# Optimization experiments

Hardware: AMD Instinct MI355X
Metric: run time of the kernel (lower is better)

## Reference

```python
import jax, jax.numpy as jnp
import numpy as np

N_SRC, N_DST, E = 65536, 16384, 262144
IN, HID, H = 256, 128, 4
N_POI, K = 100000, 50
NEG_SLOPE = 0.2


def setup_inputs() -> dict:
    key = jax.random.key(0)
    ks = jax.random.split(key, 13)
    feat = jax.random.normal(ks[0], (N_SRC, IN), jnp.float32)
    poi_cat_feat = jax.random.normal(ks[1], (N_POI, IN), jnp.float32)
    poi_coeff = jax.random.uniform(ks[2], (N_POI, K), jnp.float32)
    fc_w = jax.random.normal(ks[3], (H * HID, IN), jnp.float32) * 0.05
    attn_l = jax.random.normal(ks[4], (H, HID), jnp.float32) * 0.05
    attn_r = jax.random.normal(ks[5], (H, HID), jnp.float32) * 0.05
    bias_p = jnp.zeros((H * HID,), jnp.float32)
    res_w = jax.random.normal(ks[6], (H * HID, IN), jnp.float32) * 0.05
    w_w = jax.random.normal(ks[7], (HID, IN), jnp.float32) * 0.05
    src_idx = jax.random.randint(ks[8], (E,), 0, N_SRC)
    dst_idx = jax.random.randint(ks[9], (E,), 0, N_DST)
    output_nodes = jax.random.randint(ks[10], (N_DST,), 0, N_POI)
    neighbor_counts = jax.random.randint(ks[11], (N_POI,), 1, K + 1)
    return dict(feat=feat, poi_cat_feat=poi_cat_feat, poi_coeff=poi_coeff,
                fc_w=fc_w, attn_l=attn_l, attn_r=attn_r, bias_p=bias_p,
                res_w=res_w, w_w=w_w, src_idx=src_idx, dst_idx=dst_idx,
                output_nodes=output_nodes, neighbor_counts=neighbor_counts)


def reference(feat, poi_cat_feat, poi_coeff, fc_w, attn_l, attn_r, bias_p,
              res_w, w_w, src_idx, dst_idx, output_nodes, neighbor_counts):
    # ---- DGL GATConv on block (src -> dst), feat_drop/attn_drop = 0 (eval) ----
    feat_src = (feat @ fc_w.T).reshape(N_SRC, H, HID)        # [Nsrc,H,D]
    el = jnp.einsum('nhd,hd->nh', feat_src, attn_l)          # [Nsrc,H]
    er = jnp.einsum('nhd,hd->nh', feat_src[:N_DST], attn_r)  # [Ndst,H]
    e = jax.nn.leaky_relu(el[src_idx] + er[dst_idx], NEG_SLOPE)  # [E,H]
    # edge softmax per destination node (numerically stable)
    m = jax.ops.segment_max(e, dst_idx, num_segments=N_DST)
    m = jnp.where(jnp.isfinite(m), m, 0.0)
    ex = jnp.exp(e - m[dst_idx])
    denom = jax.ops.segment_sum(ex, dst_idx, num_segments=N_DST)
    a = ex / jnp.maximum(denom[dst_idx], 1e-9)               # [E,H]
    msgs = a[:, :, None] * feat_src[src_idx]                 # [E,H,D]
    rst = jax.ops.segment_sum(msgs, dst_idx, num_segments=N_DST)  # [Ndst,H,D]
    res = (feat[:N_DST] @ res_w.T).reshape(N_DST, H, HID)    # residual projection
    feat_gat = jax.nn.elu(rst + res + bias_p.reshape(1, H, HID))
    # ---- per-node neighbor-weighted sum: sum_j beta[nid,j] * W @ poi_cat_feat[nid],
    #      over first min(count,50) neighbors (cap-50 padded mask) ----
    cf = poi_cat_feat[output_nodes]                          # [Ndst,IN]
    valid = (jnp.arange(K)[None, :] < neighbor_counts[output_nodes][:, None])
    s = jnp.sum(poi_coeff[output_nodes] * valid.astype(cf.dtype), axis=-1)  # [Ndst]
    feat_dist = (cf @ w_w.T) * s[:, None]                    # [Ndst,HID]
    out = jax.nn.relu((feat_gat + feat_dist[:, None, :]) / 2)
    return out
```

## Files before the change

### kernel.cpp

```cpp
#include <hip/hip_runtime.h>

#define N_SRC 65536
#define N_DST 16384
#define NEDGE 262144
#define FIN 256
#define HID 128
#define KNB 50
#define NEG 0.2f
#define BCAP 64

typedef short bf8 __attribute__((ext_vector_type(8)));
typedef float f32x4 __attribute__((ext_vector_type(4)));

static __device__ __forceinline__ short f2bf(float f) {
    union { float f; unsigned u; } v; v.f = f;
    unsigned r = v.u + 0x7fffu + ((v.u >> 16) & 1u);
    return (short)(r >> 16);
}
static __device__ __forceinline__ float bf2f(short b) {
    union { unsigned u; float f; } v; v.u = ((unsigned)(unsigned short)b) << 16;
    return v.f;
}

static __device__ __forceinline__ unsigned char f2e4(float f) {
    union { float f; unsigned u; } v; v.f = f;
    unsigned s = (v.u >> 24) & 0x80u;
    v.u &= 0x7FFFFFFFu;
    v.f = fminf(v.f, 240.0f);
    unsigned u = v.u + 0x00080000u;
    int eb = (int)(u >> 23) - 120;
    if (eb < 1) return (unsigned char)s;
    unsigned m = (u >> 20) & 7u;
    return (unsigned char)(s | ((unsigned)eb << 3) | m);
}

__global__ __launch_bounds__(256) void k_prep_all(
    const float* __restrict__ feat, short* __restrict__ feat_bf,
    const float* __restrict__ fc, const float* __restrict__ rw,
    const float* __restrict__ ww, short* __restrict__ fco,
    short* __restrict__ rwo, short* __restrict__ wwo,
    const float* __restrict__ poi, const float* __restrict__ poi_coeff,
    const int* __restrict__ nodes, const int* __restrict__ ncounts,
    short* __restrict__ cf, float* __restrict__ sArr,
    const int* __restrict__ src_idx, const int* __restrict__ dst_idx,
    int* __restrict__ counts, int* __restrict__ bucket) {
    int b = blockIdx.x;
    if (b < 16384) {
        int i = b * 256 + threadIdx.x;
        float4 v = ((const float4*)feat)[i];
        short4 o; o.x = f2bf(v.x); o.y = f2bf(v.y); o.z = f2bf(v.z); o.w = f2bf(v.w);
        ((short4*)feat_bf)[i] = o;
    } else if (b < 16672) {
        int i = (b - 16384) * 256 + threadIdx.x;
        const float* src; short* dst; int off;
        if (i < 32768) { src = fc; dst = fco; off = i; }
        else if (i < 65536) { src = rw; dst = rwo; off = i - 32768; }
        else { src = ww; dst = wwo; off = i - 65536; }
        float4 v = ((const float4*)src)[off];
        short4 o; o.x = f2bf(v.x); o.y = f2bf(v.y); o.z = f2bf(v.z); o.w = f2bf(v.w);
        ((short4*)dst)[off] = o;
    } else if (b < 20768) {
        int wv = threadIdx.x >> 6, lane = threadIdx.x & 63;
        int row = (b - 16672) * 4 + wv;
        int nid = nodes[row];
        float4 v = ((const float4*)(poi + (size_t)nid * FIN))[lane];
        short4 o; o.x = f2bf(v.x); o.y = f2bf(v.y); o.z = f2bf(v.z); o.w = f2bf(v.w);
        ((short4*)(cf + (size_t)row * FIN))[lane] = o;
        int cnt = ncounts[nid];
        float s = (lane < cnt && lane < KNB) ? poi_coeff[(size_t)nid * KNB + lane] : 0.f;
        for (int m = 1; m < 64; m <<= 1) s += __shfl_xor(s, m);
        if (lane == 0) sArr[row] = s;
    } else {
        int e = (b - 20768) * 256 + threadIdx.x;
        int d = dst_idx[e];
        int pos = atomicAdd(&counts[d], 1);
        if (pos < BCAP) bucket[d * BCAP + pos] = src_idx[e];
    }
}

__global__ __launch_bounds__(256, 3) void k_gemm_all(
    const short* __restrict__ feat_bf, const short* __restrict__ fcw,
    const short* __restrict__ resw, const short* __restrict__ ww,
    const short* __restrict__ cf_bf, unsigned char* __restrict__ feat_src8,
    short* __restrict__ resO, short* __restrict__ fdist,
    const float* __restrict__ sArr, const float* __restrict__ attn_l,
    const float* __restrict__ attn_r, float* __restrict__ el, float* __restrict__ er) {
    __shared__ __align__(16) short Abuf[128 * 64];
    __shared__ __align__(16) short Bbuf[128 * 64];
    int b0 = blockIdx.x;
    int b = (b0 & 7) * 336 + (b0 >> 3);
    const short *A, *W; const float* scale = nullptr;
    short* C16 = nullptr;
    int N = 512, do_elr = 0, rowBase, colBase;
    if (b < 2048) {
        A = feat_bf; W = fcw; do_elr = 1;
        colBase = (b & 3) * 128; rowBase = (b >> 2) * 128;
    } else if (b < 2560) {
        int bb = b - 2048;
        A = feat_bf; W = resw; C16 = resO;
        colBase = (bb & 3) * 128; rowBase = (bb >> 2) * 128;
    } else {
        int bb = b - 2560;
        A = cf_bf; W = ww; C16 = fdist; scale = sArr; N = 128;
        colBase = 0; rowBase = bb * 128;
    }
    int t = threadIdx.x, wv = t >> 6, lane = t & 63;
    int l15 = lane & 15, quad = lane >> 4;
    const short* sbase = (wv < 2) ? (A + (size_t)rowBase * FIN)
                                  : (W + (size_t)colBase * FIN);
    short* dbase = (wv < 2) ? Abuf : Bbuf;
    int s0 = (wv & 1) * 8;
    int rsub = lane >> 3;
    int cg = (lane & 7) ^ rsub;

    f32x4 acc[2][8] = {};
    for (int kb = 0; kb < 4; kb++) {
#pragma unroll
        for (int q = 0; q < 8; q++) {
            int slab = s0 + q;
            int r_loc = slab * 8 + rsub;
            __builtin_amdgcn_global_load_lds(
                (const __attribute__((address_space(1))) void*)(sbase + (size_t)r_loc * FIN + kb * 64 + cg * 8),
                (__attribute__((address_space(3))) void*)(dbase + slab * 512), 16, 0, 0);
        }
        asm volatile("s_waitcnt vmcnt(0)" ::: "memory");
        __syncthreads();
#pragma unroll
        for (int kk = 0; kk < 2; kk++) {
            int gidx = (quad + kk * 4) ^ (l15 & 7);
            bf8 a[2], bfr[8];
#pragma unroll
            for (int i = 0; i < 2; i++) {
                int row = wv * 32 + i * 16 + l15;
                a[i] = *(const bf8*)(Abuf + (row * 8 + gidx) * 8);
            }
#pragma unroll
            for (int j = 0; j < 8; j++) {
                int row = j * 16 + l15;
                bfr[j] = *(const bf8*)(Bbuf + (row * 8 + gidx) * 8);
            }
#pragma unroll
            for (int i = 0; i < 2; i++)
#pragma unroll
                for (int j = 0; j < 8; j++)
                    acc[i][j] = __builtin_amdgcn_mfma_f32_16x16x32_bf16(a[i], bfr[j], acc[i][j], 0, 0, 0);
        }
        if (kb < 3) __syncthreads();
    }
#pragma unroll
    for (int i = 0; i < 2; i++)
#pragma unroll
        for (int r = 0; r < 4; r++) {
            int row = rowBase + wv * 32 + i * 16 + quad * 4 + r;
            if (do_elr) {
#pragma unroll
                for (int j = 0; j < 8; j++)
                    feat_src8[(size_t)row * 512 + colBase + j * 16 + l15] = f2e4(acc[i][j][r]);
            } else {
                float sc = scale ? scale[row] : 1.0f;
#pragma unroll
                for (int j = 0; j < 8; j++)
                    C16[(size_t)row * N + colBase + j * 16 + l15] = f2bf(acc[i][j][r] * sc);
            }
        }
    if (do_elr) {
        int h = colBase >> 7;
        float alv[8], arv[8];
#pragma unroll
        for (int j = 0; j < 8; j++) {
            alv[j] = attn_l[h * HID + j * 16 + l15];
            arv[j] = attn_r[h * HID + j * 16 + l15];
        }
#pragma unroll
        for (int i = 0; i < 2; i++)
#pragma unroll
            for (int r = 0; r < 4; r++) {
                float dl = 0.f, dr = 0.f;
#pragma unroll
                for (int j = 0; j < 8; j++) {
                    float c = acc[i][j][r];
                    dl += c * alv[j];
                    dr += c * arv[j];
                }
                dl += __shfl_xor(dl, 1); dr += __shfl_xor(dr, 1);
                dl += __shfl_xor(dl, 2); dr += __shfl_xor(dr, 2);
                dl += __shfl_xor(dl, 4); dr += __shfl_xor(dr, 4);
                dl += __shfl_xor(dl, 8); dr += __shfl_xor(dr, 8);
                if (l15 == 0) {
                    int row = rowBase + wv * 32 + i * 16 + quad * 4 + r;
                    el[row * 4 + h] = dl;
                    if (row < N_DST) er[row * 4 + h] = dr;
                }
            }
    }
}

__global__ __launch_bounds__(256) void k_agg(const int* __restrict__ counts,
                                             const int* __restrict__ bucket,
                                             const float* __restrict__ el,
                                             const float* __restrict__ er,
                                             const unsigned char* __restrict__ feat_src8,
                                             const short* __restrict__ res,
                                             const float* __restrict__ bias,
                                             const short* __restrict__ fdist,
                                             float* __restrict__ out) {
    __shared__ __align__(16) float aSm[4][256];
    __shared__ int sSm[4][64];
    int wv = threadIdx.x >> 6, lane = threadIdx.x & 63;
    int d = blockIdx.x * 4 + wv;
    int cnt = counts[d]; cnt = cnt < BCAP ? cnt : BCAP;
    float4 erv = *(const float4*)(er + (size_t)d * 4);

    int srow = 0;
    float v0 = -1e30f, v1 = -1e30f, v2 = -1e30f, v3 = -1e30f;
    if (lane < cnt) {
        srow = bucket[d * BCAP + lane];
        float4 lv = *(const float4*)(el + (size_t)srow * 4);
        v0 = lv.x + erv.x; v0 = v0 > 0 ? v0 : NEG * v0;
        v1 = lv.y + erv.y; v1 = v1 > 0 ? v1 : NEG * v1;
        v2 = lv.z + erv.z; v2 = v2 > 0 ? v2 : NEG * v2;
        v3 = lv.w + erv.w; v3 = v3 > 0 ? v3 : NEG * v3;
    }
    float m0 = v0, m1 = v1, m2 = v2, m3 = v3;
    for (int sh = 1; sh < 64; sh <<= 1) {
        m0 = fmaxf(m0, __shfl_xor(m0, sh)); m1 = fmaxf(m1, __shfl_xor(m1, sh));
        m2 = fmaxf(m2, __shfl_xor(m2, sh)); m3 = fmaxf(m3, __shfl_xor(m3, sh));
    }
    float e0 = 0.f, e1 = 0.f, e2 = 0.f, e3 = 0.f;
    if (lane < cnt) {
        e0 = __expf(v0 - m0); e1 = __expf(v1 - m1);
        e2 = __expf(v2 - m2); e3 = __expf(v3 - m3);
    }
    float s0 = e0, s1 = e1, s2 = e2, s3 = e3;
    for (int sh = 1; sh < 64; sh <<= 1) {
        s0 += __shfl_xor(s0, sh); s1 += __shfl_xor(s1, sh);
        s2 += __shfl_xor(s2, sh); s3 += __shfl_xor(s3, sh);
    }
    const float S = 0x1p120f;
    float i0 = S / fmaxf(s0, 1e-9f), i1 = S / fmaxf(s1, 1e-9f);
    float i2 = S / fmaxf(s2, 1e-9f), i3 = S / fmaxf(s3, 1e-9f);
    *(float4*)&aSm[wv][lane * 4] = make_float4(e0 * i0, e1 * i1, e2 * i2, e3 * i3);
    sSm[wv][lane] = srow;
    asm volatile("s_waitcnt lgkmcnt(0)" ::: "memory");

    int myh = lane >> 4, col0 = lane * 8;
    float acc[8] = {0.f, 0.f, 0.f, 0.f, 0.f, 0.f, 0.f, 0.f};
    for (int c = 0; c < cnt; c++) {
        int srw = sSm[wv][c];
        float afs = aSm[wv][c * 4 + myh];
        const unsigned char* p = feat_src8 + ((size_t)srw << 9) + col0;
        uint2 w8 = *(const uint2*)p;
#pragma unroll
        for (int j = 0; j < 4; j++) {
            unsigned blo = (w8.x >> (8 * j)) & 0xFFu;
            unsigned bhi = (w8.y >> (8 * j)) & 0xFFu;
            union { unsigned u; float f; } xl, xh;
            xl.u = ((blo & 0x80u) << 24) | ((blo & 0x7Fu) << 20);
            xh.u = ((bhi & 0x80u) << 24) | ((bhi & 0x7Fu) << 20);
            acc[j]     = fmaf(afs, xl.f, acc[j]);
            acc[j + 4] = fmaf(afs, xh.f, acc[j + 4]);
        }
    }

    bf8 rv = *(const bf8*)(res + (size_t)d * 512 + col0);
    float4 bv0 = *(const float4*)(bias + col0);
    float4 bv1 = *(const float4*)(bias + col0 + 4);
    float bb[8] = {bv0.x, bv0.y, bv0.z, bv0.w, bv1.x, bv1.y, bv1.z, bv1.w};
    bf8 fv = *(const bf8*)(fdist + (size_t)d * HID + (col0 & 127));
    float o[8];
#pragma unroll
    for (int j = 0; j < 8; j++) {
        float g = acc[j] + bf2f(rv[j]) + bb[j];
        g = g > 0 ? g : expm1f(g);
        float v = (g + bf2f(fv[j])) * 0.5f;
        o[j] = v > 0 ? v : 0.f;
    }
    float* op = out + (size_t)d * 512 + col0;
    *(float4*)op = make_float4(o[0], o[1], o[2], o[3]);
    *(float4*)(op + 4) = make_float4(o[4], o[5], o[6], o[7]);
}

extern "C" void kernel_launch(void* const* d_in, const int* in_sizes, int n_in,
                              void* d_out, int out_size, void* d_ws, size_t ws_size,
                              hipStream_t stream) {
    const float* feat      = (const float*)d_in[0];
    const float* poi_cat   = (const float*)d_in[1];
    const float* poi_coeff = (const float*)d_in[2];
    const float* fc_w      = (const float*)d_in[3];
    const float* attn_l    = (const float*)d_in[4];
    const float* attn_r    = (const float*)d_in[5];
    const float* bias_p    = (const float*)d_in[6];
    const float* res_w     = (const float*)d_in[7];
    const float* w_w       = (const float*)d_in[8];
    const int* src_idx     = (const int*)d_in[9];
    const int* dst_idx     = (const int*)d_in[10];
    const int* out_nodes   = (const int*)d_in[11];
    const int* ncounts     = (const int*)d_in[12];
    float* out = (float*)d_out;

    char* w = (char*)d_ws;
    auto alloc = [&](size_t bytes) -> char* {
        char* p = w; w += (bytes + 255) & ~(size_t)255; return p;
    };
    short* feat_bf  = (short*)alloc((size_t)N_SRC * FIN * 2);
    short* fcw_bf   = (short*)alloc((size_t)512 * FIN * 2);
    short* resw_bf  = (short*)alloc((size_t)512 * FIN * 2);
    short* ww_bf    = (short*)alloc((size_t)HID * FIN * 2);
    short* cf_bf    = (short*)alloc((size_t)N_DST * FIN * 2);
    unsigned char* feat_src8 = (unsigned char*)alloc((size_t)N_SRC * 512);
    short* res      = (short*)alloc((size_t)N_DST * 512 * 2);
    short* fdist    = (short*)alloc((size_t)N_DST * HID * 2);
    float* el       = (float*)alloc((size_t)N_SRC * 4 * 4);
    float* er       = (float*)alloc((size_t)N_DST * 4 * 4);
    float* sArr     = (float*)alloc((size_t)N_DST * 4);
    int* counts     = (int*)alloc((size_t)N_DST * 4);
    int* bucket     = (int*)alloc((size_t)N_DST * BCAP * 4);

    hipMemsetAsync(counts, 0, N_DST * 4, stream);

    k_prep_all<<<21792, 256, 0, stream>>>(feat, feat_bf, fc_w, res_w, w_w,
                                          fcw_bf, resw_bf, ww_bf,
                                          poi_cat, poi_coeff, out_nodes, ncounts,
                                          cf_bf, sArr, src_idx, dst_idx,
                                          counts, bucket);

    k_gemm_all<<<2688, 256, 0, stream>>>(feat_bf, fcw_bf, resw_bf, ww_bf, cf_bf,
                                         feat_src8, res, fdist, sArr,
                                         attn_l, attn_r, el, er);

    k_agg<<<N_DST / 4, 256, 0, stream>>>(counts, bucket, el, er,
                                         feat_src8, res, bias_p, fdist, out);
}
```

Before: 308.0 us.

## Fuse memset, prep, GEMM and aggregation into one cooperative persistent kernel

Replaces the memset plus three separate kernel launches with a single cooperative persistent kernel. It sizes the grid to resident capacity, loops each block over virtual block indices, and separates the phases with grid-wide syncs. This is meant to remove launch overhead and inter-kernel gaps and tail drain. In exchange it adds grid.sync costs, and the persistent loops may balance work less well than hardware scheduling. A fallback path keeps the original multi-kernel launches if the cooperative launch is unavailable.

Measured after the change: 305.3 us. About the same (-0.9%).

```diff
diff --git a/kernel.cpp b/kernel.cpp
--- a/kernel.cpp
+++ b/kernel.cpp
@@ -1,4 +1,7 @@
 #include <hip/hip_runtime.h>
+#include <hip/hip_cooperative_groups.h>
+
+namespace cgrp = cooperative_groups;
 
 #define N_SRC 65536
 #define N_DST 16384
@@ -34,84 +37,77 @@
     return (unsigned char)(s | ((unsigned)eb << 3) | m);
 }
 
-__global__ __launch_bounds__(256) void k_prep_all(
-    const float* __restrict__ feat, short* __restrict__ feat_bf,
-    const float* __restrict__ fc, const float* __restrict__ rw,
-    const float* __restrict__ ww, short* __restrict__ fco,
-    short* __restrict__ rwo, short* __restrict__ wwo,
-    const float* __restrict__ poi, const float* __restrict__ poi_coeff,
-    const int* __restrict__ nodes, const int* __restrict__ ncounts,
-    short* __restrict__ cf, float* __restrict__ sArr,
-    const int* __restrict__ src_idx, const int* __restrict__ dst_idx,
-    int* __restrict__ counts, int* __restrict__ bucket) {
-    int b = blockIdx.x;
-    if (b < 16384) {
-        int i = b * 256 + threadIdx.x;
-        float4 v = ((const float4*)feat)[i];
+struct MegaP {
+    const float *feat, *poi, *coeff, *attnl, *attnr, *bias;
+    const float *fc32, *rw32, *ww32;
+    const int *src, *dst, *nodes, *ncnt;
+    short *feat_bf, *fcw, *resw, *ww, *cf;
+    unsigned char *fsrc8;
+    short *res, *fdist;
+    float *el, *er, *sArr, *out;
+    int *counts, *bucket;
+};
+
+
+static __device__ __forceinline__ void dev_prep(int vb, int t, const MegaP& P) {
+    if (vb < 16384) {
+        int i = vb * 256 + t;
+        float4 v = ((const float4*)P.feat)[i];
         short4 o; o.x = f2bf(v.x); o.y = f2bf(v.y); o.z = f2bf(v.z); o.w = f2bf(v.w);
-        ((short4*)feat_bf)[i] = o;
-    } else if (b < 16672) {
-        int i = (b - 16384) * 256 + threadIdx.x;
+        ((short4*)P.feat_bf)[i] = o;
+    } else if (vb < 16672) {
+        int i = (vb - 16384) * 256 + t;
         const float* src; short* dst; int off;
-        if (i < 32768) { src = fc; dst = fco; off = i; }
-        else if (i < 65536) { src = rw; dst = rwo; off = i - 32768; }
-        else { src = ww; dst = wwo; off = i - 65536; }
+        if (i < 32768) { src = P.fc32; dst = P.fcw; off = i; }
+        else if (i < 65536) { src = P.rw32; dst = P.resw; off = i - 32768; }
+        else { src = P.ww32; dst = P.ww; off = i - 65536; }
         float4 v = ((const float4*)src)[off];
         short4 o; o.x = f2bf(v.x); o.y = f2bf(v.y); o.z = f2bf(v.z); o.w = f2bf(v.w);
         ((short4*)dst)[off] = o;
-    } else if (b < 20768) {
-        int wv = threadIdx.x >> 6, lane = threadIdx.x & 63;
-        int row = (b - 16672) * 4 + wv;
-        int nid = nodes[row];
-        float4 v = ((const float4*)(poi + (size_t)nid * FIN))[lane];
+    } else if (vb < 20768) {
+        int wv = t >> 6, lane = t & 63;
+        int row = (vb - 16672) * 4 + wv;
+        int nid = P.nodes[row];
+        float4 v = ((const float4*)(P.poi + (size_t)nid * FIN))[lane];
         short4 o; o.x = f2bf(v.x); o.y = f2bf(v.y); o.z = f2bf(v.z); o.w = f2bf(v.w);
-        ((short4*)(cf + (size_t)row * FIN))[lane] = o;
-        int cnt = ncounts[nid];
-        float s = (lane < cnt && lane < KNB) ? poi_coeff[(size_t)nid * KNB + lane] : 0.f;
+        ((short4*)(P.cf + (size_t)row * FIN))[lane] = o;
+        int cnt = P.ncnt[nid];
+        float s = (lane < cnt && lane < KNB) ? P.coeff[(size_t)nid * KNB + lane] : 0.f;
         for (int m = 1; m < 64; m <<= 1) s += __shfl_xor(s, m);
-        if (lane == 0) sArr[row] = s;
+        if (lane == 0) P.sArr[row] = s;
     } else {
-        int e = (b - 20768) * 256 + threadIdx.x;
-        int d = dst_idx[e];
-        int pos = atomicAdd(&counts[d], 1);
-        if (pos < BCAP) bucket[d * BCAP + pos] = src_idx[e];
-    }
-}
-
-__global__ __launch_bounds__(256, 3) void k_gemm_all(
-    const short* __restrict__ feat_bf, const short* __restrict__ fcw,
-    const short* __restrict__ resw, const short* __restrict__ ww,
-    const short* __restrict__ cf_bf, unsigned char* __restrict__ feat_src8,
-    short* __restrict__ resO, short* __restrict__ fdist,
-    const float* __restrict__ sArr, const float* __restrict__ attn_l,
-    const float* __restrict__ attn_r, float* __restrict__ el, float* __restrict__ er) {
-    __shared__ __align__(16) short Abuf[128 * 64];
-    __shared__ __align__(16) short Bbuf[128 * 64];
-    int b0 = blockIdx.x;
-    int b = (b0 & 7) * 336 + (b0 >> 3);
+        int e = (vb - 20768) * 256 + t;
+        int d = P.dst[e];
+        int pos = atomicAdd(&P.counts[d], 1);
+        if (pos < BCAP) P.bucket[d * BCAP + pos] = P.src[e];
+    }
+}
+
+static __device__ __forceinline__ void dev_gemm_tile(
+    int b, int t, const MegaP& P, short* Abuf, short* Bbuf) {
     const short *A, *W; const float* scale = nullptr;
     short* C16 = nullptr;
     int N = 512, do_elr = 0, rowBase, colBase;
     if (b < 2048) {
-        A = feat_bf; W = fcw; do_elr = 1;
+        A = P.feat_bf; W = P.fcw; do_elr = 1;
         colBase = (b & 3) * 128; rowBase = (b >> 2) * 128;
     } else if (b < 2560) {
         int bb = b - 2048;
-        A = feat_bf; W = resw; C16 = resO;
+        A = P.feat_bf; W = P.resw; C16 = P.res;
         colBase = (bb & 3) * 128; rowBase = (bb >> 2) * 128;
     } else {
         int bb = b - 2560;
-        A = cf_bf; W = ww; C16 = fdist; scale = sArr; N = 128;
+        A = P.cf; W = P.ww; C16 = P.fdist; scale = P.sArr; N = 128;
         colBase = 0; rowBase = bb * 128;
     }
-    int t = threadIdx.x, wv = t >> 6, lane = t & 63;
+    int wv = t >> 6, lane = t & 63;
     int l15 = lane & 15, quad = lane >> 4;
+    int s0 = (wv & 1) * 8;
+    int rsub = lane >> 3;
+    int cgn = (lane & 7) ^ rsub;
     const short* sbase = (wv < 2) ? (A + (size_t)rowBase * FIN)
                                   : (W + (size_t)colBase * FIN);
     short* dbase = (wv < 2) ? Abuf : Bbuf;
-    int s0 = (wv & 1) * 8;
-    int rsub = lane >> 3;
-    int cg = (lane & 7) ^ rsub;
 
     f32x4 acc[2][8] = {};
     for (int kb = 0; kb < 4; kb++) {
@@ -120,7 +116,7 @@
             int slab = s0 + q;
             int r_loc = slab * 8 + rsub;
             __builtin_amdgcn_global_load_lds(
-                (const __attribute__((address_space(1))) void*)(sbase + (size_t)r_loc * FIN + kb * 64 + cg * 8),
+                (const __attribute__((address_space(1))) void*)(sbase + (size_t)r_loc * FIN + kb * 64 + cgn * 8),
                 (__attribute__((address_space(3))) void*)(dbase + slab * 512), 16, 0, 0);
         }
         asm volatile("s_waitcnt vmcnt(0)" ::: "memory");
@@ -155,7 +151,7 @@
             if (do_elr) {
 #pragma unroll
                 for (int j = 0; j < 8; j++)
-                    feat_src8[(size_t)row * 512 + colBase + j * 16 + l15] = f2e4(acc[i][j][r]);
+                    P.fsrc8[(size_t)row * 512 + colBase + j * 16 + l15] = f2e4(acc[i][j][r]);
             } else {
                 float sc = scale ? scale[row] : 1.0f;
 #pragma unroll
@@ -168,8 +164,8 @@
         float alv[8], arv[8];
 #pragma unroll
         for (int j = 0; j < 8; j++) {
-            alv[j] = attn_l[h * HID + j * 16 + l15];
-            arv[j] = attn_r[h * HID + j * 16 + l15];
+            alv[j] = P.attnl[h * HID + j * 16 + l15];
+            arv[j] = P.attnr[h * HID + j * 16 + l15];
         }
 #pragma unroll
         for (int i = 0; i < 2; i++)
@@ -188,34 +184,23 @@
                 dl += __shfl_xor(dl, 8); dr += __shfl_xor(dr, 8);
                 if (l15 == 0) {
                     int row = rowBase + wv * 32 + i * 16 + quad * 4 + r;
-                    el[row * 4 + h] = dl;
-                    if (row < N_DST) er[row * 4 + h] = dr;
+                    P.el[row * 4 + h] = dl;
+                    if (row < N_DST) P.er[row * 4 + h] = dr;
                 }
             }
     }
 }
 
-__global__ __launch_bounds__(256) void k_agg(const int* __restrict__ counts,
-                                             const int* __restrict__ bucket,
-                                             const float* __restrict__ el,
-                                             const float* __restrict__ er,
-                                             const unsigned char* __restrict__ feat_src8,
-                                             const short* __restrict__ res,
-                                             const float* __restrict__ bias,
-                                             const short* __restrict__ fdist,
-                                             float* __restrict__ out) {
-    __shared__ __align__(16) float aSm[4][256];
-    __shared__ int sSm[4][64];
-    int wv = threadIdx.x >> 6, lane = threadIdx.x & 63;
-    int d = blockIdx.x * 4 + wv;
-    int cnt = counts[d]; cnt = cnt < BCAP ? cnt : BCAP;
-    float4 erv = *(const float4*)(er + (size_t)d * 4);
+static __device__ __forceinline__ void dev_agg_one(
+    int d, int lane, const MegaP& P, float* aW, int* sW) {
+    int cnt = P.counts[d]; cnt = cnt < BCAP ? cnt : BCAP;
+    float4 erv = *(const float4*)(P.er + (size_t)d * 4);
 
     int srow = 0;
     float v0 = -1e30f, v1 = -1e30f, v2 = -1e30f, v3 = -1e30f;
     if (lane < cnt) {
-        srow = bucket[d * BCAP + lane];
-        float4 lv = *(const float4*)(el + (size_t)srow * 4);
+        srow = P.bucket[d * BCAP + lane];
+        float4 lv = *(const float4*)(P.el + (size_t)srow * 4);
         v0 = lv.x + erv.x; v0 = v0 > 0 ? v0 : NEG * v0;
         v1 = lv.y + erv.y; v1 = v1 > 0 ? v1 : NEG * v1;
         v2 = lv.z + erv.z; v2 = v2 > 0 ? v2 : NEG * v2;
@@ -239,16 +224,16 @@
     const float S = 0x1p120f;
     float i0 = S / fmaxf(s0, 1e-9f), i1 = S / fmaxf(s1, 1e-9f);
     float i2 = S / fmaxf(s2, 1e-9f), i3 = S / fmaxf(s3, 1e-9f);
-    *(float4*)&aSm[wv][lane * 4] = make_float4(e0 * i0, e1 * i1, e2 * i2, e3 * i3);
-    sSm[wv][lane] = srow;
+    *(float4*)&aW[lane * 4] = make_float4(e0 * i0, e1 * i1, e2 * i2, e3 * i3);
+    sW[lane] = srow;
     asm volatile("s_waitcnt lgkmcnt(0)" ::: "memory");
 
     int myh = lane >> 4, col0 = lane * 8;
     float acc[8] = {0.f, 0.f, 0.f, 0.f, 0.f, 0.f, 0.f, 0.f};
     for (int c = 0; c < cnt; c++) {
-        int srw = sSm[wv][c];
-        float afs = aSm[wv][c * 4 + myh];
-        const unsigned char* p = feat_src8 + ((size_t)srw << 9) + col0;
+        int srw = sW[c];
+        float afs = aW[c * 4 + myh];
+        const unsigned char* p = P.fsrc8 + ((size_t)srw << 9) + col0;
         uint2 w8 = *(const uint2*)p;
 #pragma unroll
         for (int j = 0; j < 4; j++) {
@@ -262,11 +247,11 @@
         }
     }
 
-    bf8 rv = *(const bf8*)(res + (size_t)d * 512 + col0);
-    float4 bv0 = *(const float4*)(bias + col0);
-    float4 bv1 = *(const float4*)(bias + col0 + 4);
+    bf8 rv = *(const bf8*)(P.res + (size_t)d * 512 + col0);
+    float4 bv0 = *(const float4*)(P.bias + col0);
+    float4 bv1 = *(const float4*)(P.bias + col0 + 4);
     float bb[8] = {bv0.x, bv0.y, bv0.z, bv0.w, bv1.x, bv1.y, bv1.z, bv1.w};
-    bf8 fv = *(const bf8*)(fdist + (size_t)d * HID + (col0 & 127));
+    bf8 fv = *(const bf8*)(P.fdist + (size_t)d * HID + (col0 & 127));
     float o[8];
 #pragma unroll
     for (int j = 0; j < 8; j++) {
@@ -275,59 +260,114 @@
         float v = (g + bf2f(fv[j])) * 0.5f;
         o[j] = v > 0 ? v : 0.f;
     }
-    float* op = out + (size_t)d * 512 + col0;
+    float* op = P.out + (size_t)d * 512 + col0;
     *(float4*)op = make_float4(o[0], o[1], o[2], o[3]);
     *(float4*)(op + 4) = make_float4(o[4], o[5], o[6], o[7]);
+}
+
+__global__ __launch_bounds__(256, 3) void k_mega(MegaP P) {
+    __shared__ __align__(16) char smem[32768];
+    cgrp::grid_group grid = cgrp::this_grid();
+    int t = threadIdx.x;
+    int nb = gridDim.x;
+
+    for (int i = blockIdx.x * 256 + t; i < N_DST; i += nb * 256)
+        P.counts[i] = 0;
+    grid.sync();
+
+    for (int vb = blockIdx.x; vb < 21792; vb += nb)
+        dev_prep(vb, t, P);
+    grid.sync();
+
+    {
+        short* Abuf = (short*)smem;
+        short* Bbuf = (short*)(smem + 16384);
+        int xcd = blockIdx.x & 7, lix = blockIdx.x >> 3, nw = nb >> 3;
+        for (int ti = lix; ti < 336; ti += nw) {
+            dev_gemm_tile(xcd * 336 + ti, t, P, Abuf, Bbuf);
+            __syncthreads();
+        }
+    }
+    grid.sync();
+
+    {
+        float* aSm = (float*)smem;
+        int* sSm = (int*)(smem + 4096);
+        int wv = t >> 6, lane = t & 63;
+        float* aW = aSm + wv * 256;
+        int* sW = sSm + wv * 64;
+        for (int d = blockIdx.x * 4 + wv; d < N_DST; d += nb * 4)
+            dev_agg_one(d, lane, P, aW, sW);
+    }
+}
+
+__global__ __launch_bounds__(256) void k_prep(MegaP P) {
+    dev_prep(blockIdx.x, threadIdx.x, P);
+}
+__global__ __launch_bounds__(256, 3) void k_gemm(MegaP P) {
+    __shared__ __align__(16) short Abuf[128 * 64];
+    __shared__ __align__(16) short Bbuf[128 * 64];
+    int b0 = blockIdx.x;
+    dev_gemm_tile((b0 & 7) * 336 + (b0 >> 3), threadIdx.x, P, Abuf, Bbuf);
+}
+__global__ __launch_bounds__(256) void k_agg2(MegaP P) {
+    __shared__ __align__(16) float aSm[4][256];
+    __shared__ int sSm[4][64];
+    int wv = threadIdx.x >> 6, lane = threadIdx.x & 63;
+    dev_agg_one(blockIdx.x * 4 + wv, lane, P, aSm[wv], sSm[wv]);
 }
 
 extern "C" void kernel_launch(void* const* d_in, const int* in_sizes, int n_in,
                               void* d_out, int out_size, void* d_ws, size_t ws_size,
                               hipStream_t stream) {
-    const float* feat      = (const float*)d_in[0];
-    const float* poi_cat   = (const float*)d_in[1];
-    const float* poi_coeff = (const float*)d_in[2];
-    const float* fc_w      = (const float*)d_in[3];
-    const float* attn_l    = (const float*)d_in[4];
-    const float* attn_r    = (const float*)d_in[5];
-    const float* bias_p    = (const float*)d_in[6];
-    const float* res_w     = (const float*)d_in[7];
-    const float* w_w       = (const float*)d_in[8];
-    const int* src_idx     = (const int*)d_in[9];
-    const int* dst_idx     = (const int*)d_in[10];
-    const int* out_nodes   = (const int*)d_in[11];
-    const int* ncounts     = (const int*)d_in[12];
-    float* out = (float*)d_out;
-
     char* w = (char*)d_ws;
     auto alloc = [&](size_t bytes) -> char* {
         char* p = w; w += (bytes + 255) & ~(size_t)255; return p;
     };
-    short* feat_bf  = (short*)alloc((size_t)N_SRC * FIN * 2);
-    short* fcw_bf   = (short*)alloc((size_t)512 * FIN * 2);
-    short* resw_bf  = (short*)alloc((size_t)512 * FIN * 2);
-    short* ww_bf    = (short*)alloc((size_t)HID * FIN * 2);
-    short* cf_bf    = (short*)alloc((size_t)N_DST * FIN * 2);
-    unsigned char* feat_src8 = (unsigned char*)alloc((size_t)N_SRC * 512);
-    short* res      = (short*)alloc((size_t)N_DST * 512 * 2);
-    short* fdist    = (short*)alloc((size_t)N_DST * HID * 2);
-    float* el       = (float*)alloc((size_t)N_SRC * 4 * 4);
-    float* er       = (float*)alloc((size_t)N_DST * 4 * 4);
-    float* sArr     = (float*)alloc((size_t)N_DST * 4);
-    int* counts     = (int*)alloc((size_t)N_DST * 4);
-    int* bucket     = (int*)alloc((size_t)N_DST * BCAP * 4);
-
-    hipMemsetAsync(counts, 0, N_DST * 4, stream);
-
-    k_prep_all<<<21792, 256, 0, stream>>>(feat, feat_bf, fc_w, res_w, w_w,
-                                          fcw_bf, resw_bf, ww_bf,
-                                          poi_cat, poi_coeff, out_nodes, ncounts,
-                                          cf_bf, sArr, src_idx, dst_idx,
-                                          counts, bucket);
-
-    k_gemm_all<<<2688, 256, 0, stream>>>(feat_bf, fcw_bf, resw_bf, ww_bf, cf_bf,
-                                         feat_src8, res, fdist, sArr,
-                                         attn_l, attn_r, el, er);
-
-    k_agg<<<N_DST / 4, 256, 0, stream>>>(counts, bucket, el, er,
-                                         feat_src8, res, bias_p, fdist, out);
-}
+    MegaP P;
+    P.feat  = (const float*)d_in[0];
+    P.poi   = (const float*)d_in[1];
+    P.coeff = (const float*)d_in[2];
+    P.fc32  = (const float*)d_in[3];
+    P.attnl = (const float*)d_in[4];
+    P.attnr = (const float*)d_in[5];
+    P.bias  = (const float*)d_in[6];
+    P.rw32  = (const float*)d_in[7];
+    P.ww32  = (const float*)d_in[8];
+    P.src   = (const int*)d_in[9];
+    P.dst   = (const int*)d_in[10];
+    P.nodes = (const int*)d_in[11];
+    P.ncnt  = (const int*)d_in[12];
+    P.out   = (float*)d_out;
+
+    P.feat_bf = (short*)alloc((size_t)N_SRC * FIN * 2);
+    P.fcw     = (short*)alloc((size_t)512 * FIN * 2);
+    P.resw    = (short*)alloc((size_t)512 * FIN * 2);
+    P.ww      = (short*)alloc((size_t)HID * FIN * 2);
+    P.cf      = (short*)alloc((size_t)N_DST * FIN * 2);
+    P.fsrc8   = (unsigned char*)alloc((size_t)N_SRC * 512);
+    P.res     = (short*)alloc((size_t)N_DST * 512 * 2);
+    P.fdist   = (short*)alloc((size_t)N_DST * HID * 2);
+    P.el      = (float*)alloc((size_t)N_SRC * 4 * 4);
+    P.er      = (float*)alloc((size_t)N_DST * 4 * 4);
+    P.sArr    = (float*)alloc((size_t)N_DST * 4);
+    P.counts  = (int*)alloc((size_t)N_DST * 4);
+    P.bucket  = (int*)alloc((size_t)N_DST * BCAP * 4);
+
+    int maxb = 0;
+    hipError_t qrc = hipOccupancyMaxActiveBlocksPerMultiprocessor(
+        &maxb, (const void*)k_mega, 256, 0);
+    if (qrc == hipSuccess && maxb >= 2) {
+        int bpc = maxb < 3 ? maxb : 3;
+        dim3 grid(256 * bpc);
+        void* args[] = { (void*)&P };
+        hipError_t rc = hipLaunchCooperativeKernel((const void*)k_mega, grid,
+                                                   dim3(256), args, 0, stream);
+        if (rc == hipSuccess) return;
+    }
+
+    hipMemsetAsync(P.counts, 0, N_DST * 4, stream);
+    k_prep<<<21792, 256, 0, stream>>>(P);
+    k_gemm<<<2688, 256, 0, stream>>>(P);
+    k_agg2<<<N_DST / 4, 256, 0, stream>>>(P);
+}
```
